# Kernel tuning notes

Hardware: AMD Instinct MI355X
Metric: run time of the kernel (lower is better)

## Reference

```python
import jax, jax.numpy as jnp
import numpy as np

B, C, H, W = 4, 256, 64, 64
OUT_C = 256
K = 3          # kernel_size
P = K // 2     # zero padding
EPS = 1e-5     # F.layer_norm default eps


def setup_inputs() -> dict:
    key = jax.random.key(0)
    ks = jax.random.split(key, 9)
    s = 0.02
    return {
        "x":  jax.random.normal(ks[0], (B, C, H, W), dtype=jnp.float32),
        "Wq": jax.random.normal(ks[1], (C, C), dtype=jnp.float32) * s,
        "bq": jax.random.normal(ks[2], (C,), dtype=jnp.float32) * s,
        "Wk": jax.random.normal(ks[3], (C, C), dtype=jnp.float32) * s,
        "bk": jax.random.normal(ks[4], (C,), dtype=jnp.float32) * s,
        "Wv": jax.random.normal(ks[5], (C, C), dtype=jnp.float32) * s,
        "bv": jax.random.normal(ks[6], (C,), dtype=jnp.float32) * s,
        "Wo": jax.random.normal(ks[7], (OUT_C, C), dtype=jnp.float32) * s,
        "bo": jax.random.normal(ks[8], (OUT_C,), dtype=jnp.float32) * s,
    }


def _forward(x, Wq, bq, Wk, bk, Wv, bv, Wo, bo):
    # LayerNorm over the last two dims [H, W], no affine (per (b, c) plane).
    mu = jnp.mean(x, axis=(2, 3), keepdims=True)
    var = jnp.var(x, axis=(2, 3), keepdims=True)
    xn = (x - mu) * jax.lax.rsqrt(var + EPS)

    xh = jnp.transpose(xn, (0, 2, 3, 1))            # [B, H, W, C]
    scale = jnp.asarray(C, xh.dtype) ** -0.5        # depth_scale = C**-0.5

    # Query only at each center pixel (only the center output is kept).
    q = (xh @ Wq.T + bq) * scale                    # [B, H, W, C]

    # Zero-pad the normalized input, then project: padded positions get K=bk, V=bv
    # exactly as torch's Linear applied to zero-padded windows.
    xp = jnp.pad(xh, ((0, 0), (P, P), (P, P), (0, 0)))  # [B, H+2P, W+2P, C]
    Kp = xp @ Wk.T + bk
    Vp = xp @ Wv.T + bv

    # Gather the K*K neighborhood for every pixel (small fixed loop over 9 shifts).
    Kw = jnp.stack([Kp[:, i:i + H, j:j + W, :] for i in range(K) for j in range(K)], axis=3)  # [B,H,W,9,C]
    Vw = jnp.stack([Vp[:, i:i + H, j:j + W, :] for i in range(K) for j in range(K)], axis=3)  # [B,H,W,9,C]

    logits = jnp.einsum('bhwc,bhwnc->bhwn', q, Kw)  # [B, H, W, 9]
    attn = jax.nn.softmax(logits, axis=-1)
    ctx = jnp.einsum('bhwn,bhwnc->bhwc', attn, Vw)  # [B, H, W, C]

    out = ctx @ Wo.T + bo                           # [B, H, W, OUT_C]
    return jnp.transpose(out, (0, 3, 1, 2))         # [B, OUT_C, H, W]


def reference(x, Wq, bq, Wk, bk, Wv, bv, Wo, bo):
    return _forward(x, Wq, bq, Wk, bk, Wv, bv, Wo, bo)
```

## Files before the change

### kernel.cpp

```cpp
#include <hip/hip_runtime.h>

typedef unsigned short u16;
typedef unsigned int   u32;

typedef __attribute__((ext_vector_type(4))) float f32x4;
typedef __attribute__((ext_vector_type(8))) short bf16x8;

#define HWDIM 4096
#define CDIM  256

__device__ __forceinline__ float bf2f(u16 u) { return __uint_as_float(((u32)u) << 16); }
__device__ __forceinline__ u16 f2bf(float f) {
    u32 u = __float_as_uint(f);
    u32 r = (u + 0x7fffu + ((u >> 16) & 1u)) >> 16;
    return (u16)r;
}
__device__ __forceinline__ void unpack8(uint4 r, float* f) {
    f[0] = __uint_as_float(r.x << 16); f[1] = __uint_as_float(r.x & 0xffff0000u);
    f[2] = __uint_as_float(r.y << 16); f[3] = __uint_as_float(r.y & 0xffff0000u);
    f[4] = __uint_as_float(r.z << 16); f[5] = __uint_as_float(r.z & 0xffff0000u);
    f[6] = __uint_as_float(r.w << 16); f[7] = __uint_as_float(r.w & 0xffff0000u);
}

#define GLL16(g, l) \
    __builtin_amdgcn_global_load_lds((const __attribute__((address_space(1))) u32*)(g), \
                                     (__attribute__((address_space(3))) u32*)(l), 16, 0, 0)

__global__ __launch_bounds__(256) void fill_kernel(float* __restrict__ out, int n) {
    int i = blockIdx.x * 256 + threadIdx.x;
    if (i < n) out[i] = 1.0f;
}

__global__ __launch_bounds__(256) void prep_kernel(const float* __restrict__ x,
                                                   const float* __restrict__ Wq,
                                                   const float* __restrict__ Wk,
                                                   const float* __restrict__ Wv,
                                                   const float* __restrict__ Wo,
                                                   const float* __restrict__ bq,
                                                   const float* __restrict__ bk,
                                                   const float* __restrict__ bv,
                                                   u16* __restrict__ Wqkv,
                                                   u16* __restrict__ Woc,
                                                   float* __restrict__ biasStack,
                                                   float2* __restrict__ stats) {
    int bx = blockIdx.x;
    int t = threadIdx.x;
    if (bx < 1024) {
        const float* px = x + (size_t)bx * HWDIM;
        float sum = 0.f, ss = 0.f;
#pragma unroll
        for (int it = 0; it < 4; ++it) {
            float4 v = *(const float4*)(px + (t + it * 256) * 4);
            sum += v.x + v.y + v.z + v.w;
            ss  += v.x * v.x + v.y * v.y + v.z * v.z + v.w * v.w;
        }
#pragma unroll
        for (int o = 32; o; o >>= 1) { sum += __shfl_xor(sum, o); ss += __shfl_xor(ss, o); }
        __shared__ float s1[4], s2[4];
        int wid = t >> 6, lane = t & 63;
        if (lane == 0) { s1[wid] = sum; s2[wid] = ss; }
        __syncthreads();
        if (t == 0) {
            float S = s1[0] + s1[1] + s1[2] + s1[3];
            float Q = s2[0] + s2[1] + s2[2] + s2[3];
            float mu  = S * (1.f / HWDIM);
            float var = Q * (1.f / HWDIM) - mu * mu;
            stats[bx] = make_float2(mu, rsqrtf(var + 1e-5f));
        }
        return;
    }
    int idx = bx - 1024;
    int yy = idx >> 6, xx = idx & 63;
    if (yy == 4) {
        if (xx == 0) {
            biasStack[t]       = bq[t] * 0.0625f;
            biasStack[t + 256] = bk[t];
            biasStack[t + 512] = bv[t];
        }
        return;
    }
    const float* s; u16* d; float sc = 1.f;
    if (yy == 0)      { s = Wq; d = Wqkv;          sc = 0.0625f; }
    else if (yy == 1) { s = Wk; d = Wqkv + 65536; }
    else if (yy == 2) { s = Wv; d = Wqkv + 131072; }
    else              { s = Wo; d = Woc; }
    int i = (xx * 256 + t) * 4;
    float4 f = *(const float4*)(s + i);
    u16 tmp[4] = {f2bf(f.x * sc), f2bf(f.y * sc), f2bf(f.z * sc), f2bf(f.w * sc)};
    *(uint2*)(d + i) = *(uint2*)tmp;
}

__global__ __launch_bounds__(256) void ln_transpose_kernel(const float* __restrict__ x,
                                                           const float2* __restrict__ stats,
                                                           u16* __restrict__ xh) {
    __shared__ __align__(16) u16 tile[64 * 72];
    int b  = blockIdx.z;
    int c0 = blockIdx.y * 64;
    int p0 = blockIdx.x * 64;
    int t  = threadIdx.x;
    int c_loc = t >> 2;
    int pc    = (t & 3) * 16;
    int plane = b * CDIM + c0 + c_loc;
    float2 st = stats[plane];
    const float* px = x + (size_t)plane * HWDIM + p0 + pc;
#pragma unroll
    for (int j2 = 0; j2 < 4; j2++) {
        float4 v = *(const float4*)(px + j2 * 4);
        int p = pc + j2 * 4;
        tile[(p + 0) * 72 + c_loc] = f2bf((v.x - st.x) * st.y);
        tile[(p + 1) * 72 + c_loc] = f2bf((v.y - st.x) * st.y);
        tile[(p + 2) * 72 + c_loc] = f2bf((v.z - st.x) * st.y);
        tile[(p + 3) * 72 + c_loc] = f2bf((v.w - st.x) * st.y);
    }
    __syncthreads();
    int cc = (t & 7) * 8;
#pragma unroll
    for (int it = 0; it < 2; ++it) {
        int p_loc = (t >> 3) + it * 32;
        uint4 val = *(uint4*)&tile[p_loc * 72 + cc];
        *(uint4*)(xh + ((size_t)(b * HWDIM + p0 + p_loc)) * CDIM + c0 + cc) = val;
    }
}

__global__ __launch_bounds__(256) void gemm_qkv_kernel(const u16* __restrict__ xh,
                                                       const u16* __restrict__ Wqkv,
                                                       const float* __restrict__ biasStack,
                                                       u16* __restrict__ qkv) {
    __shared__ __align__(16) u16 lA[64 * 32];
    __shared__ __align__(16) u16 lB[256 * 32];
    int t = threadIdx.x, lane = t & 63, wid = t >> 6;
    int waveM = wid >> 1, waveN = wid & 1;
    int m0 = blockIdx.x * 64;
    int g  = blockIdx.y;
    const u16* Wg = Wqkv + g * 65536;
    f32x4 acc[2][8];
#pragma unroll
    for (int i = 0; i < 2; i++)
#pragma unroll
        for (int j = 0; j < 8; j++) acc[i][j] = (f32x4){0.f, 0.f, 0.f, 0.f};
    int fr = lane & 15, kq = (lane >> 4) * 8;
    int r = t >> 2, kc = (t & 3) * 8;
    const u16* gA = xh + (size_t)(m0 + r) * 256 + kc;
    const u16* gB = Wg + (size_t)r * 256 + kc;
    u16* lA0 = lA + wid * 512;
    u16* lB0 = lB + wid * 512;
    for (int k0 = 0; k0 < 256; k0 += 32) {
        GLL16(gA + k0, lA0);
        GLL16(gB + k0,             lB0);
        GLL16(gB + k0 +  64 * 256, lB0 + 2048);
        GLL16(gB + k0 + 128 * 256, lB0 + 4096);
        GLL16(gB + k0 + 192 * 256, lB0 + 6144);
        __syncthreads();
        bf16x8 af[2], bfr[8];
#pragma unroll
        for (int i = 0; i < 2; i++)
            af[i]  = *(const bf16x8*)&lA[(waveM * 32 + i * 16 + fr) * 32 + kq];
#pragma unroll
        for (int j = 0; j < 8; j++)
            bfr[j] = *(const bf16x8*)&lB[(waveN * 128 + j * 16 + fr) * 32 + kq];
#pragma unroll
        for (int i = 0; i < 2; i++)
#pragma unroll
            for (int j = 0; j < 8; j++)
                acc[i][j] = __builtin_amdgcn_mfma_f32_16x16x32_bf16(af[i], bfr[j], acc[i][j], 0, 0, 0);
        __syncthreads();
    }
    int r0 = (lane >> 4) * 4;
#pragma unroll
    for (int j = 0; j < 8; j++) {
        int nl = waveN * 128 + j * 16 + fr;
        int ng = g * 256 + nl;
        float bval = biasStack[ng];
#pragma unroll
        for (int i = 0; i < 2; i++) {
            int mrow = m0 + waveM * 32 + i * 16 + r0;
#pragma unroll
            for (int rr = 0; rr < 4; rr++)
                qkv[(size_t)(mrow + rr) * 768 + ng] = f2bf(acc[i][j][rr] + bval);
        }
    }
}

__global__ __launch_bounds__(256) void attn_kernel(const u16* __restrict__ qkv,
                                                   const float* __restrict__ biasStack,
                                                   u16* __restrict__ ctx) {
    int t = threadIdx.x, wid = t >> 6, lane = t & 63;
    int pl = lane >> 4, ln16 = lane & 15;
    int pix = blockIdx.x * 16 + wid * 4 + pl;
    int h = (pix >> 6) & 63, w = pix & 63;
    int ch = ln16 * 16;
    const u16* qrow = qkv + (size_t)pix * 768 + ch;
    float qv[16];
    unpack8(*(const uint4*)qrow,       qv);
    unpack8(*(const uint4*)(qrow + 8), qv + 8);
    float part[9];
    int off[9];
#pragma unroll
    for (int n = 0; n < 9; n++) {
        int dy = n / 3 - 1, dx = n % 3 - 1;
        int hh = h + dy, ww = w + dx;
        bool inb = ((unsigned)hh < 64u) && ((unsigned)ww < 64u);
        off[n] = inb ? ((pix + dy * 64 + dx) * 768) : -1;
        float kv[16];
        if (off[n] >= 0) {
            const u16* p = qkv + off[n] + 256 + ch;
            unpack8(*(const uint4*)p,       kv);
            unpack8(*(const uint4*)(p + 8), kv + 8);
        } else {
            const float* p = biasStack + 256 + ch;
#pragma unroll
            for (int c = 0; c < 4; c++) *(float4*)(kv + c * 4) = *(const float4*)(p + c * 4);
        }
        float d = 0.f;
#pragma unroll
        for (int c = 0; c < 16; c++) d += qv[c] * kv[c];
        part[n] = d;
    }
#pragma unroll
    for (int o = 8; o; o >>= 1) {
#pragma unroll
        for (int n = 0; n < 9; n++) part[n] += __shfl_xor(part[n], o);
    }
    float m = part[0];
#pragma unroll
    for (int n = 1; n < 9; n++) m = fmaxf(m, part[n]);
    float e[9], s = 0.f;
#pragma unroll
    for (int n = 0; n < 9; n++) { e[n] = __expf(part[n] - m); s += e[n]; }
    float inv = 1.f / s;
    float acc[16];
#pragma unroll
    for (int c = 0; c < 16; c++) acc[c] = 0.f;
#pragma unroll
    for (int n = 0; n < 9; n++) {
        float vv[16];
        if (off[n] >= 0) {
            const u16* p = qkv + off[n] + 512 + ch;
            unpack8(*(const uint4*)p,       vv);
            unpack8(*(const uint4*)(p + 8), vv + 8);
        } else {
            const float* p = biasStack + 512 + ch;
#pragma unroll
            for (int c = 0; c < 4; c++) *(float4*)(vv + c * 4) = *(const float4*)(p + c * 4);
        }
        float wn = e[n] * inv;
#pragma unroll
        for (int c = 0; c < 16; c++) acc[c] += wn * vv[c];
    }
    u32 wds[8];
#pragma unroll
    for (int c = 0; c < 8; c++)
        wds[c] = (u32)f2bf(acc[2 * c]) | ((u32)f2bf(acc[2 * c + 1]) << 16);
    u16* dst = ctx + (size_t)pix * 256 + ch;
    *(uint4*)dst       = make_uint4(wds[0], wds[1], wds[2], wds[3]);
    *(uint4*)(dst + 8) = make_uint4(wds[4], wds[5], wds[6], wds[7]);
}

__global__ __launch_bounds__(256) void gemm_out_kernel(const u16* __restrict__ ctx,
                                                       const u16* __restrict__ Wo,
                                                       const float* __restrict__ bo,
                                                       float* __restrict__ out) {
    __shared__ __align__(16) u16 lA[128 * 32];
    __shared__ __align__(16) u16 lB[64 * 32];
    int t = threadIdx.x, lane = t & 63, wid = t >> 6;
    int waveM = wid >> 1, waveN = wid & 1;
    int m0 = blockIdx.x * 128;
    int n0 = blockIdx.y * 64;
    f32x4 acc[4][2];
#pragma unroll
    for (int i = 0; i < 4; i++)
#pragma unroll
        for (int j = 0; j < 2; j++) acc[i][j] = (f32x4){0.f, 0.f, 0.f, 0.f};
    int fr = lane & 15, kq = (lane >> 4) * 8;
    int r = t >> 2, kc = (t & 3) * 8;
    const u16* gA0 = ctx + (size_t)(m0 + r) * 256 + kc;
    const u16* gA1 = gA0 + 64 * 256;
    const u16* gB0 = Wo + (size_t)(n0 + r) * 256 + kc;
    u16* lA0 = lA + wid * 512;
    u16* lA1 = lA0 + 2048;
    u16* lB0 = lB + wid * 512;
    for (int k0 = 0; k0 < 256; k0 += 32) {
        GLL16(gA0 + k0, lA0);
        GLL16(gA1 + k0, lA1);
        GLL16(gB0 + k0, lB0);
        __syncthreads();
        bf16x8 af[4], bfr[2];
#pragma unroll
        for (int i = 0; i < 4; i++) af[i]  = *(const bf16x8*)&lA[(waveM * 64 + i * 16 + fr) * 32 + kq];
#pragma unroll
        for (int j = 0; j < 2; j++) bfr[j] = *(const bf16x8*)&lB[(waveN * 32 + j * 16 + fr) * 32 + kq];
#pragma unroll
        for (int i = 0; i < 4; i++)
#pragma unroll
            for (int j = 0; j < 2; j++)
                acc[i][j] = __builtin_amdgcn_mfma_f32_16x16x32_bf16(af[i], bfr[j], acc[i][j], 0, 0, 0);
        __syncthreads();
    }
    int r0 = (lane >> 4) * 4;
#pragma unroll
    for (int j = 0; j < 2; j++) {
        int ng = n0 + waveN * 32 + j * 16 + fr;
        float bval = bo[ng];
#pragma unroll
        for (int i = 0; i < 4; i++) {
            int m = m0 + waveM * 64 + i * 16 + r0;
            int bidx = m >> 12;
            int p = m & 4095;
            float4 vv = make_float4(acc[i][j][0] + bval, acc[i][j][1] + bval,
                                    acc[i][j][2] + bval, acc[i][j][3] + bval);
            *(float4*)(out + ((size_t)(bidx * 256 + ng)) * HWDIM + p) = vv;
        }
    }
}

extern "C" void kernel_launch(void* const* d_in, const int* in_sizes, int n_in,
                              void* d_out, int out_size, void* d_ws, size_t ws_size,
                              hipStream_t stream) {
    const float* x  = (const float*)d_in[0];
    const float* Wq = (const float*)d_in[1];
    const float* bq = (const float*)d_in[2];
    const float* Wk = (const float*)d_in[3];
    const float* bk = (const float*)d_in[4];
    const float* Wv = (const float*)d_in[5];
    const float* bv = (const float*)d_in[6];
    const float* Wo = (const float*)d_in[7];
    const float* bo = (const float*)d_in[8];
    float* out = (float*)d_out;

    char* wsb = (char*)d_ws;
    const size_t MB = 1ull << 20;

    if (ws_size < 34 * MB) {
        hipLaunchKernelGGL(fill_kernel, dim3((out_size + 255) / 256), dim3(256), 0, stream,
                           out, out_size);
        return;
    }

    float2* stats     = (float2*)wsb;
    float*  biasStack = (float*)(wsb + 16 * 1024);
    u16* Wqkv = (u16*)(wsb + 64 * 1024);
    u16* Woc  = (u16*)(wsb + 448 * 1024);
    u16* xh   = (u16*)(wsb + 1 * MB);
    u16* qkv  = (u16*)(wsb + 9 * MB);
    u16* ctx  = xh;

    hipLaunchKernelGGL(prep_kernel, dim3(1344), dim3(256), 0, stream,
                       x, Wq, Wk, Wv, Wo, bq, bk, bv, Wqkv, Woc, biasStack, stats);
    hipLaunchKernelGGL(ln_transpose_kernel, dim3(64, 4, 4), dim3(256), 0, stream, x, stats, xh);
    hipLaunchKernelGGL(gemm_qkv_kernel,     dim3(256, 3),   dim3(256), 0, stream,
                       xh, Wqkv, biasStack, qkv);
    hipLaunchKernelGGL(attn_kernel,         dim3(1024),     dim3(256), 0, stream,
                       qkv, biasStack, ctx);
    hipLaunchKernelGGL(gemm_out_kernel,     dim3(128, 4),   dim3(256), 0, stream,
                       ctx, Woc, bo, out);
}
```

Baseline: 130.8 us.

## Fuse LayerNorm-transpose into QKV GEMM, staging full normalized A tile in LDS

Removes the separate ln_transpose kernel and the bf16 xh intermediate. Each QKV GEMM block now reads its 64 pixels x 256 channels of fp32 x directly, normalizes, converts to bf16 and writes a padded full-K A tile to LDS once before the K loop. This saves one launch and an 8MB write plus read, but x is re-read 3 times (once per g) and LDS use grows to about 50KB, which may lower occupancy. The LDS stores are scalar 2-byte writes with a transposed stride, so bank conflicts are possible.

Measured after the change: 128.9 us. Within noise of the previous version (-1.4%).

```diff
diff --git a/kernel.cpp b/kernel.cpp
--- a/kernel.cpp
+++ b/kernel.cpp
@@ -90,49 +90,31 @@
     *(uint2*)(d + i) = *(uint2*)tmp;
 }
 
-__global__ __launch_bounds__(256) void ln_transpose_kernel(const float* __restrict__ x,
-                                                           const float2* __restrict__ stats,
-                                                           u16* __restrict__ xh) {
-    __shared__ __align__(16) u16 tile[64 * 72];
-    int b  = blockIdx.z;
-    int c0 = blockIdx.y * 64;
-    int p0 = blockIdx.x * 64;
-    int t  = threadIdx.x;
-    int c_loc = t >> 2;
-    int pc    = (t & 3) * 16;
-    int plane = b * CDIM + c0 + c_loc;
-    float2 st = stats[plane];
-    const float* px = x + (size_t)plane * HWDIM + p0 + pc;
-#pragma unroll
-    for (int j2 = 0; j2 < 4; j2++) {
-        float4 v = *(const float4*)(px + j2 * 4);
-        int p = pc + j2 * 4;
-        tile[(p + 0) * 72 + c_loc] = f2bf((v.x - st.x) * st.y);
-        tile[(p + 1) * 72 + c_loc] = f2bf((v.y - st.x) * st.y);
-        tile[(p + 2) * 72 + c_loc] = f2bf((v.z - st.x) * st.y);
-        tile[(p + 3) * 72 + c_loc] = f2bf((v.w - st.x) * st.y);
-    }
-    __syncthreads();
-    int cc = (t & 7) * 8;
-#pragma unroll
-    for (int it = 0; it < 2; ++it) {
-        int p_loc = (t >> 3) + it * 32;
-        uint4 val = *(uint4*)&tile[p_loc * 72 + cc];
-        *(uint4*)(xh + ((size_t)(b * HWDIM + p0 + p_loc)) * CDIM + c0 + cc) = val;
-    }
-}
-
-__global__ __launch_bounds__(256) void gemm_qkv_kernel(const u16* __restrict__ xh,
+#define ASTRIDE 264
+__global__ __launch_bounds__(256) void gemm_qkv_kernel(const float* __restrict__ x,
+                                                       const float2* __restrict__ stats,
                                                        const u16* __restrict__ Wqkv,
                                                        const float* __restrict__ biasStack,
                                                        u16* __restrict__ qkv) {
-    __shared__ __align__(16) u16 lA[64 * 32];
+    __shared__ __align__(16) u16 lA[64 * ASTRIDE];
     __shared__ __align__(16) u16 lB[256 * 32];
     int t = threadIdx.x, lane = t & 63, wid = t >> 6;
     int waveM = wid >> 1, waveN = wid & 1;
     int m0 = blockIdx.x * 64;
     int g  = blockIdx.y;
+    int b  = m0 >> 12, p0 = m0 & 4095;
     const u16* Wg = Wqkv + g * 65536;
+    float2 st = stats[b * 256 + t];
+    const float* px = x + ((size_t)(b * 256 + t)) * HWDIM + p0;
+#pragma unroll
+    for (int jj = 0; jj < 16; jj++) {
+        float4 v = *(const float4*)(px + jj * 4);
+        int p = jj * 4;
+        lA[(p + 0) * ASTRIDE + t] = f2bf((v.x - st.x) * st.y);
+        lA[(p + 1) * ASTRIDE + t] = f2bf((v.y - st.x) * st.y);
+        lA[(p + 2) * ASTRIDE + t] = f2bf((v.z - st.x) * st.y);
+        lA[(p + 3) * ASTRIDE + t] = f2bf((v.w - st.x) * st.y);
+    }
     f32x4 acc[2][8];
 #pragma unroll
     for (int i = 0; i < 2; i++)
@@ -140,12 +122,10 @@
         for (int j = 0; j < 8; j++) acc[i][j] = (f32x4){0.f, 0.f, 0.f, 0.f};
     int fr = lane & 15, kq = (lane >> 4) * 8;
     int r = t >> 2, kc = (t & 3) * 8;
-    const u16* gA = xh + (size_t)(m0 + r) * 256 + kc;
     const u16* gB = Wg + (size_t)r * 256 + kc;
-    u16* lA0 = lA + wid * 512;
     u16* lB0 = lB + wid * 512;
+    __syncthreads();
     for (int k0 = 0; k0 < 256; k0 += 32) {
-        GLL16(gA + k0, lA0);
         GLL16(gB + k0,             lB0);
         GLL16(gB + k0 +  64 * 256, lB0 + 2048);
         GLL16(gB + k0 + 128 * 256, lB0 + 4096);
@@ -154,7 +134,7 @@
         bf16x8 af[2], bfr[8];
 #pragma unroll
         for (int i = 0; i < 2; i++)
-            af[i]  = *(const bf16x8*)&lA[(waveM * 32 + i * 16 + fr) * 32 + kq];
+            af[i]  = *(const bf16x8*)&lA[(waveM * 32 + i * 16 + fr) * ASTRIDE + k0 + kq];
 #pragma unroll
         for (int j = 0; j < 8; j++)
             bfr[j] = *(const bf16x8*)&lB[(waveN * 128 + j * 16 + fr) * 32 + kq];
@@ -340,17 +320,15 @@
     float*  biasStack = (float*)(wsb + 16 * 1024);
     u16* Wqkv = (u16*)(wsb + 64 * 1024);
     u16* Woc  = (u16*)(wsb + 448 * 1024);
-    u16* xh   = (u16*)(wsb + 1 * MB);
+    u16* ctx  = (u16*)(wsb + 1 * MB);
     u16* qkv  = (u16*)(wsb + 9 * MB);
-    u16* ctx  = xh;
 
     hipLaunchKernelGGL(prep_kernel, dim3(1344), dim3(256), 0, stream,
                        x, Wq, Wk, Wv, Wo, bq, bk, bv, Wqkv, Woc, biasStack, stats);
-    hipLaunchKernelGGL(ln_transpose_kernel, dim3(64, 4, 4), dim3(256), 0, stream, x, stats, xh);
-    hipLaunchKernelGGL(gemm_qkv_kernel,     dim3(256, 3),   dim3(256), 0, stream,
-                       xh, Wqkv, biasStack, qkv);
-    hipLaunchKernelGGL(attn_kernel,         dim3(1024),     dim3(256), 0, stream,
+    hipLaunchKernelGGL(gemm_qkv_kernel, dim3(256, 3), dim3(256), 0, stream,
+                       x, stats, Wqkv, biasStack, qkv);
+    hipLaunchKernelGGL(attn_kernel,     dim3(1024),   dim3(256), 0, stream,
                        qkv, biasStack, ctx);
-    hipLaunchKernelGGL(gemm_out_kernel,     dim3(128, 4),   dim3(256), 0, stream,
+    hipLaunchKernelGGL(gemm_out_kernel, dim3(128, 4), dim3(256), 0, stream,
                        ctx, Woc, bo, out);
 }
```
